# Performance work log

Hardware: AMD Instinct MI355X
Metric: run time of the kernel (lower is better)

Reference implementation:

```python
import jax, jax.numpy as jnp
import numpy as np

ENS, S_DIM, A_DIM, R_DIM, HID, LAYER_NUM = 7, 30, 8, 1, 200, 5
N_HID_LAYERS = LAYER_NUM - 2  # hidden->hidden Linear+Swish blocks


def swish(x):
    return x * jax.nn.sigmoid(x)


def setup_inputs() -> dict:
    key = jax.random.key(0)
    ks = jax.random.split(key, 14)
    N = 32768
    out_dim = S_DIM + R_DIM
    s = jax.random.normal(ks[0], (N, ENS, S_DIM), dtype=jnp.float32)
    a = jax.random.normal(ks[1], (N, ENS, A_DIM), dtype=jnp.float32)
    sc = 0.05
    W1 = jax.random.normal(ks[2], (ENS, S_DIM + A_DIM, HID), dtype=jnp.float32) * sc
    b1 = jax.random.normal(ks[3], (ENS, HID), dtype=jnp.float32) * sc
    Wh = jax.random.normal(ks[4], (N_HID_LAYERS, ENS, HID, HID), dtype=jnp.float32) * sc
    bh = jax.random.normal(ks[5], (N_HID_LAYERS, ENS, HID), dtype=jnp.float32) * sc
    Wmu = jax.random.normal(ks[6], (ENS, HID, out_dim), dtype=jnp.float32) * sc
    bmu = jax.random.normal(ks[7], (ENS, out_dim), dtype=jnp.float32) * sc
    Wsig = jax.random.normal(ks[8], (ENS, HID, out_dim), dtype=jnp.float32) * sc
    bsig = jax.random.normal(ks[9], (ENS, out_dim), dtype=jnp.float32) * sc
    max_lv_s = jnp.ones((1, S_DIM), dtype=jnp.float32) / 2.0
    min_lv_s = jnp.ones((1, S_DIM), dtype=jnp.float32) * -10.0
    max_lv_r = jnp.ones((1, R_DIM), dtype=jnp.float32) / 2.0
    min_lv_r = jnp.ones((1, R_DIM), dtype=jnp.float32) * -10.0
    return {"s": s, "a": a, "W1": W1, "b1": b1, "Wh": Wh, "bh": bh,
            "Wmu": Wmu, "bmu": bmu, "Wsig": Wsig, "bsig": bsig,
            "max_lv_s": max_lv_s, "min_lv_s": min_lv_s,
            "max_lv_r": max_lv_r, "min_lv_r": min_lv_r}


def reference(s, a, W1, b1, Wh, bh, Wmu, bmu, Wsig, bsig,
              max_lv_s, min_lv_s, max_lv_r, min_lv_r):
    # x: [N, E, s+a]; per-ensemble-member weights batched along E
    x = jnp.concatenate([s, a], axis=-1)
    h = swish(jnp.einsum('ned,edh->neh', x, W1) + b1)
    for i in range(Wh.shape[0]):
        h = swish(jnp.einsum('neh,ehk->nek', h, Wh[i]) + bh[i])
    mu = jnp.einsum('neh,eho->neo', h, Wmu) + bmu      # [N, E, s+r]
    sigma = jnp.einsum('neh,eho->neo', h, Wsig) + bsig  # raw logvar/2
    ds_mu, r_mu = mu[..., :S_DIM], mu[..., S_DIM:]
    ds_sg, r_sg = sigma[..., :S_DIM], sigma[..., S_DIM:]
    # soft clamping of log-variance, then exp
    ds_sg = (max_lv_s - jax.nn.softplus(max_lv_s - 2.0 * ds_sg)) / 2.0
    ds_sg = (min_lv_s + jax.nn.softplus(2.0 * ds_sg - min_lv_s)) / 2.0
    ds_sg = jnp.exp(ds_sg)
    r_sg = (max_lv_r - jax.nn.softplus(max_lv_r - 2.0 * r_sg)) / 2.0
    r_sg = (min_lv_r + jax.nn.softplus(2.0 * r_sg - min_lv_r)) / 2.0
    r_sg = jnp.exp(r_sg)
    return ((ds_mu, ds_sg), (r_mu, r_sg))
```

## Files before the change

### kernel.cpp

```cpp
#include <hip/hip_runtime.h>
#include <hip/hip_bf16.h>

#define ENS 7
#define SDIM 30
#define ADIM 8
#define DIN 38
#define HID 200
#define DOUT 31
#define NHL 3
#define HS 232
#define MT 64

typedef __bf16 bf16x8 __attribute__((ext_vector_type(8)));
typedef float f32x4 __attribute__((ext_vector_type(4)));

#define U_L1 13312
#define U_H 46592
#define OFF_HD2 (U_L1 + NHL * U_H)
#define PER_E (OFF_HD2 + 14336)
#define WS_TOTAL (ENS * PER_E)

__device__ __forceinline__ unsigned short f2bf(float f) {
    unsigned u = __float_as_uint(f);
    u += 0x7fffu + ((u >> 16) & 1u);
    return (unsigned short)(u >> 16);
}

__device__ __forceinline__ unsigned pk2(float a, float b) {
    __hip_bfloat162 h = __float22bfloat162_rn(make_float2(a, b));
    return *reinterpret_cast<unsigned*>(&h);
}

__device__ __forceinline__ float softplusf(float x) {
    return fmaxf(x, 0.f) + __logf(1.f + __expf(-fabsf(x)));
}

__global__ void prep_kernel(const float* __restrict__ W1, const float* __restrict__ Wh,
                            const float* __restrict__ Wmu, const float* __restrict__ Wsig,
                            unsigned short* __restrict__ ws) {
    int idx = blockIdx.x * 256 + threadIdx.x;
    if (idx >= WS_TOTAL) return;
    int e = idx / PER_E, r = idx % PER_E;
    int j = r & 7, lane = (r >> 3) & 63;
    int l16 = lane & 15, q = lane >> 4;
    float v = 0.f;
    if (r < U_L1) {
        int fi = r >> 9;
        int ct = fi >> 1, st = fi & 1;
        int k = st * 32 + q * 8 + j, n = ct * 16 + l16;
        if (k < DIN && n < HID) v = W1[(e * DIN + k) * HID + n];
    } else if (r < OFF_HD2) {
        int rh = r - U_L1;
        int l = rh / U_H, r2 = rh % U_H;
        int fi = r2 >> 9;
        int ct = fi / 7, st = fi % 7;
        int k = st * 32 + q * 8 + j, n = ct * 16 + l16;
        if (k < HID && n < HID) v = Wh[((l * ENS + e) * HID + (long)k) * HID + n];
    } else {
        int r2 = r - OFF_HD2;
        int fi = r2 >> 9;
        int ct = fi / 7, st = fi % 7;
        int k = st * 32 + q * 8 + j, n = ct * 16 + l16;
        if (k < HID) {
            if (n < DOUT) v = Wmu[(e * HID + k) * DOUT + n];
            else if (n >= 32 && n < 32 + DOUT) v = Wsig[(e * HID + k) * DOUT + (n - 32)];
        }
    }
    ws[idx] = f2bf(v);
}

template<int S, int NT>
__device__ __forceinline__ void runLayer(const unsigned short* __restrict__ gB,
                                         const unsigned short* hA,
                                         int wv, int lane, int l16, int quad,
                                         f32x4 acc[4][4]) {
#pragma unroll
    for (int r = 0; r < 4; r++)
#pragma unroll
        for (int j = 0; j < 4; j++) acc[r][j] = (f32x4){0.f, 0.f, 0.f, 0.f};

    const unsigned short* fp = gB + lane * 8;
    bf16x8 bcur[4], bnxt[4];
#pragma unroll
    for (int j = 0; j < 4; j++) {
        int ct = wv + 4 * j;
        if (ct < NT) bcur[j] = *((const bf16x8*)(fp + (ct * S) * 512));
    }
#pragma unroll
    for (int st = 0; st < S; ++st) {
        if (st + 1 < S) {
#pragma unroll
            for (int j = 0; j < 4; j++) {
                int ct = wv + 4 * j;
                if (ct < NT) bnxt[j] = *((const bf16x8*)(fp + (ct * S + st + 1) * 512));
            }
        }
        bf16x8 af[4];
#pragma unroll
        for (int r = 0; r < 4; r++)
            af[r] = *((const bf16x8*)(hA + (r * 16 + l16) * HS + st * 32 + quad * 8));
#pragma unroll
        for (int j = 0; j < 4; j++) {
            int ct = wv + 4 * j;
            if (ct < NT) {
#pragma unroll
                for (int r = 0; r < 4; r++)
                    acc[r][j] = __builtin_amdgcn_mfma_f32_16x16x32_bf16(bcur[j], af[r], acc[r][j], 0, 0, 0);
            }
        }
#pragma unroll
        for (int j = 0; j < 4; j++) bcur[j] = bnxt[j];
    }
}

__launch_bounds__(256, 3)
__global__ void ens_mlp_kernel(const float* __restrict__ s, const float* __restrict__ a,
                               const float* __restrict__ b1, const float* __restrict__ bh,
                               const float* __restrict__ bmu, const float* __restrict__ bsig,
                               const float* __restrict__ maxs, const float* __restrict__ mins,
                               const float* __restrict__ maxr, const float* __restrict__ minr,
                               const unsigned short* __restrict__ ws,
                               float* __restrict__ out, int N) {
    __shared__ unsigned short hA[MT * HS];

    const int tid = threadIdx.x;
    const int wv = tid >> 6, lane = tid & 63;
    const int quad = lane >> 4, l16 = lane & 15;
    const int bid = blockIdx.x;
    const int e = bid % ENS, n0 = (bid / ENS) * MT;

    for (int i = tid; i < MT * HS / 8; i += 256) ((uint4*)hA)[i] = make_uint4(0, 0, 0, 0);
    __syncthreads();

    {
        int m = tid & 63, cg = tid >> 6;
        long g = n0 + m;
        const float* srow = s + (g * ENS + e) * SDIM;
        const float* arow = a + (g * ENS + e) * ADIM;
#pragma unroll
        for (int k = 0; k < 10; k++) {
            int c = cg * 10 + k;
            if (c < DIN) {
                float v = (c < SDIM) ? srow[c] : arow[c - SDIM];
                hA[m * HS + c] = f2bf(v);
            }
        }
    }
    __syncthreads();

    f32x4 acc[4][4];

    auto epiH = [&](const float* bias) {
#pragma unroll
        for (int j = 0; j < 4; j++) {
            int ct = wv + 4 * j;
            if (ct < 13) {
                int col = ct * 16 + quad * 4;
                float4 bc4 = make_float4(0.f, 0.f, 0.f, 0.f);
                if (col < HID) bc4 = *((const float4*)(bias + col));
#pragma unroll
                for (int r = 0; r < 4; r++) {
                    int row = r * 16 + l16;
                    float v0 = acc[r][j][0] + bc4.x, v1 = acc[r][j][1] + bc4.y;
                    float v2 = acc[r][j][2] + bc4.z, v3 = acc[r][j][3] + bc4.w;
                    v0 *= __builtin_amdgcn_rcpf(1.f + __expf(-v0));
                    v1 *= __builtin_amdgcn_rcpf(1.f + __expf(-v1));
                    v2 *= __builtin_amdgcn_rcpf(1.f + __expf(-v2));
                    v3 *= __builtin_amdgcn_rcpf(1.f + __expf(-v3));
                    *((uint2*)(hA + row * HS + col)) = make_uint2(pk2(v0, v1), pk2(v2, v3));
                }
            }
        }
    };

    const unsigned short* we = ws + e * PER_E;

    runLayer<2, 13>(we, hA, wv, lane, l16, quad, acc);
    __syncthreads();
    epiH(b1 + e * HID);
    __syncthreads();
#pragma unroll
    for (int l = 0; l < NHL; l++) {
        runLayer<7, 13>(we + U_L1 + l * U_H, hA, wv, lane, l16, quad, acc);
        __syncthreads();
        epiH(bh + (l * ENS + e) * HID);
        __syncthreads();
    }
    runLayer<7, 4>(we + OFF_HD2, hA, wv, lane, l16, quad, acc);

    const long off1 = (long)N * ENS * SDIM;
    const long off2 = 2 * off1;
    const long off3 = off2 + (long)N * ENS;
    {
        const bool isSig = (wv >= 2);
        const int c0 = (wv & 1) * 16 + quad * 4;
        float bias_i[4], mx_i[4], mn_i[4];
#pragma unroll
        for (int i = 0; i < 4; i++) {
            int c = c0 + i;
            bias_i[i] = (c < DOUT) ? (isSig ? bsig : bmu)[e * DOUT + c] : 0.f;
            if (isSig) {
                mx_i[i] = (c < SDIM) ? maxs[c] : maxr[0];
                mn_i[i] = (c < SDIM) ? mins[c] : minr[0];
            }
        }
#pragma unroll
        for (int r = 0; r < 4; r++) {
            long g = n0 + r * 16 + l16;
            long rowbase = (g * ENS + e) * SDIM;
#pragma unroll
            for (int i = 0; i < 4; i++) {
                int c = c0 + i;
                if (c < DOUT) {
                    float v = acc[r][0][i] + bias_i[i];
                    if (!isSig) {
                        if (c < SDIM) out[rowbase + c] = v;
                        else out[off2 + g * ENS + e] = v;
                    } else {
                        v = 0.5f * (mx_i[i] - softplusf(mx_i[i] - 2.f * v));
                        v = 0.5f * (mn_i[i] + softplusf(2.f * v - mn_i[i]));
                        v = __expf(v);
                        if (c < SDIM) out[off1 + rowbase + c] = v;
                        else out[off3 + g * ENS + e] = v;
                    }
                }
            }
        }
    }
}

extern "C" void kernel_launch(void* const* d_in, const int* in_sizes, int n_in,
                              void* d_out, int out_size, void* d_ws, size_t ws_size,
                              hipStream_t stream) {
    const float* s    = (const float*)d_in[0];
    const float* a    = (const float*)d_in[1];
    const float* W1   = (const float*)d_in[2];
    const float* b1   = (const float*)d_in[3];
    const float* Wh   = (const float*)d_in[4];
    const float* bh   = (const float*)d_in[5];
    const float* Wmu  = (const float*)d_in[6];
    const float* bmu  = (const float*)d_in[7];
    const float* Wsig = (const float*)d_in[8];
    const float* bsig = (const float*)d_in[9];
    const float* maxs = (const float*)d_in[10];
    const float* mins = (const float*)d_in[11];
    const float* maxr = (const float*)d_in[12];
    const float* minr = (const float*)d_in[13];
    float* out = (float*)d_out;
    unsigned short* ws = (unsigned short*)d_ws;

    int N = in_sizes[0] / (ENS * SDIM);

    int prepBlocks = (WS_TOTAL + 255) / 256;
    prep_kernel<<<prepBlocks, 256, 0, stream>>>(W1, Wh, Wmu, Wsig, ws);

    int mainBlocks = (N / MT) * ENS;
    ens_mlp_kernel<<<mainBlocks, 256, 0, stream>>>(s, a, b1, bh, bmu, bsig,
                                                   maxs, mins, maxr, minr, ws, out, N);
}
```

Before: 264.3 us.

## Rebalance column tiles across waves and prefetch next layer weights across boundaries

```diff
diff --git a/kernel.cpp b/kernel.cpp
--- a/kernel.cpp
+++ b/kernel.cpp
@@ -69,51 +69,53 @@
     ws[idx] = f2bf(v);
 }
 
-template<int S, int NT>
-__device__ __forceinline__ void runLayer(const unsigned short* __restrict__ gB,
+template<int S, int OWN, bool SH, int NS, int NOWN, bool NSH>
+__device__ __forceinline__ void runLayer(const unsigned short* __restrict__ fo,
+                                         const unsigned short* __restrict__ fs,
+                                         const unsigned short* __restrict__ nfo,
+                                         const unsigned short* __restrict__ nfs,
                                          const unsigned short* hA,
-                                         int wv, int lane, int l16, int quad,
-                                         f32x4 acc[4][4]) {
+                                         int swv, int l16, int quad,
+                                         f32x4 (&accO)[4][3], f32x4& accS,
+                                         bf16x8 (&bq)[4]) {
 #pragma unroll
     for (int r = 0; r < 4; r++)
 #pragma unroll
-        for (int j = 0; j < 4; j++) acc[r][j] = (f32x4){0.f, 0.f, 0.f, 0.f};
-
-    const unsigned short* fp = gB + lane * 8;
-    bf16x8 bcur[4], bnxt[4];
-#pragma unroll
-    for (int j = 0; j < 4; j++) {
-        int ct = wv + 4 * j;
-        if (ct < NT) bcur[j] = *((const bf16x8*)(fp + (ct * S) * 512));
-    }
+        for (int c = 0; c < 3; c++) accO[r][c] = (f32x4){0.f, 0.f, 0.f, 0.f};
+    accS = (f32x4){0.f, 0.f, 0.f, 0.f};
+
 #pragma unroll
     for (int st = 0; st < S; ++st) {
+        bf16x8 bn[4];
         if (st + 1 < S) {
 #pragma unroll
-            for (int j = 0; j < 4; j++) {
-                int ct = wv + 4 * j;
-                if (ct < NT) bnxt[j] = *((const bf16x8*)(fp + (ct * S + st + 1) * 512));
-            }
+            for (int c = 0; c < OWN; c++) bn[c] = *((const bf16x8*)(fo + (c * S + st + 1) * 512));
+            if (SH) bn[3] = *((const bf16x8*)(fs + (st + 1) * 512));
+        } else if (NS > 0) {
+#pragma unroll
+            for (int c = 0; c < NOWN; c++) bn[c] = *((const bf16x8*)(nfo + (c * NS) * 512));
+            if (NSH) bn[3] = *((const bf16x8*)(nfs));
         }
         bf16x8 af[4];
 #pragma unroll
         for (int r = 0; r < 4; r++)
             af[r] = *((const bf16x8*)(hA + (r * 16 + l16) * HS + st * 32 + quad * 8));
-#pragma unroll
-        for (int j = 0; j < 4; j++) {
-            int ct = wv + 4 * j;
-            if (ct < NT) {
-#pragma unroll
-                for (int r = 0; r < 4; r++)
-                    acc[r][j] = __builtin_amdgcn_mfma_f32_16x16x32_bf16(bcur[j], af[r], acc[r][j], 0, 0, 0);
-            }
-        }
-#pragma unroll
-        for (int j = 0; j < 4; j++) bcur[j] = bnxt[j];
-    }
-}
-
-__launch_bounds__(256, 3)
+        bf16x8 afs;
+        if (SH) afs = *((const bf16x8*)(hA + (swv * 16 + l16) * HS + st * 32 + quad * 8));
+#pragma unroll
+        for (int c = 0; c < OWN; c++)
+#pragma unroll
+            for (int r = 0; r < 4; r++)
+                accO[r][c] = __builtin_amdgcn_mfma_f32_16x16x32_bf16(bq[c], af[r], accO[r][c], 0, 0, 0);
+        if (SH) accS = __builtin_amdgcn_mfma_f32_16x16x32_bf16(bq[3], afs, accS, 0, 0, 0);
+        if (st + 1 < S || NS > 0) {
+#pragma unroll
+            for (int c = 0; c < 4; c++) bq[c] = bn[c];
+        }
+    }
+}
+
+__launch_bounds__(256, 4)
 __global__ void ens_mlp_kernel(const float* __restrict__ s, const float* __restrict__ a,
                                const float* __restrict__ b1, const float* __restrict__ bh,
                                const float* __restrict__ bmu, const float* __restrict__ bsig,
@@ -126,6 +128,7 @@
     const int tid = threadIdx.x;
     const int wv = tid >> 6, lane = tid & 63;
     const int quad = lane >> 4, l16 = lane & 15;
+    const int swv = __builtin_amdgcn_readfirstlane(wv);
     const int bid = blockIdx.x;
     const int e = bid % ENS, n0 = (bid / ENS) * MT;
 
@@ -148,52 +151,82 @@
     }
     __syncthreads();
 
-    f32x4 acc[4][4];
+    const unsigned short* we = ws + e * PER_E;
+    const unsigned short* L1o = we + swv * 3 * 2 * 512 + lane * 8;
+    const unsigned short* L1s = we + 12 * 2 * 512 + lane * 8;
+    const unsigned short* H0o = we + U_L1 + swv * 3 * 7 * 512 + lane * 8;
+    const unsigned short* H0s = we + U_L1 + 12 * 7 * 512 + lane * 8;
+    const unsigned short* H1o = H0o + U_H;
+    const unsigned short* H1s = H0s + U_H;
+    const unsigned short* H2o = H1o + U_H;
+    const unsigned short* H2s = H1s + U_H;
+    const unsigned short* HDo = we + OFF_HD2 + swv * 7 * 512 + lane * 8;
+
+    f32x4 accO[4][3];
+    f32x4 accS;
+    bf16x8 bq[4];
 
     auto epiH = [&](const float* bias) {
 #pragma unroll
-        for (int j = 0; j < 4; j++) {
-            int ct = wv + 4 * j;
-            if (ct < 13) {
-                int col = ct * 16 + quad * 4;
-                float4 bc4 = make_float4(0.f, 0.f, 0.f, 0.f);
-                if (col < HID) bc4 = *((const float4*)(bias + col));
-#pragma unroll
-                for (int r = 0; r < 4; r++) {
-                    int row = r * 16 + l16;
-                    float v0 = acc[r][j][0] + bc4.x, v1 = acc[r][j][1] + bc4.y;
-                    float v2 = acc[r][j][2] + bc4.z, v3 = acc[r][j][3] + bc4.w;
-                    v0 *= __builtin_amdgcn_rcpf(1.f + __expf(-v0));
-                    v1 *= __builtin_amdgcn_rcpf(1.f + __expf(-v1));
-                    v2 *= __builtin_amdgcn_rcpf(1.f + __expf(-v2));
-                    v3 *= __builtin_amdgcn_rcpf(1.f + __expf(-v3));
-                    *((uint2*)(hA + row * HS + col)) = make_uint2(pk2(v0, v1), pk2(v2, v3));
-                }
-            }
+        for (int c = 0; c < 3; c++) {
+            int col = (3 * swv + c) * 16 + quad * 4;
+            float4 bc4 = *((const float4*)(bias + col));
+#pragma unroll
+            for (int r = 0; r < 4; r++) {
+                float v0 = accO[r][c][0] + bc4.x, v1 = accO[r][c][1] + bc4.y;
+                float v2 = accO[r][c][2] + bc4.z, v3 = accO[r][c][3] + bc4.w;
+                v0 *= __builtin_amdgcn_rcpf(1.f + __expf(-v0));
+                v1 *= __builtin_amdgcn_rcpf(1.f + __expf(-v1));
+                v2 *= __builtin_amdgcn_rcpf(1.f + __expf(-v2));
+                v3 *= __builtin_amdgcn_rcpf(1.f + __expf(-v3));
+                *((uint2*)(hA + (r * 16 + l16) * HS + col)) = make_uint2(pk2(v0, v1), pk2(v2, v3));
+            }
+        }
+        {
+            int col = 192 + quad * 4;
+            float4 bc4 = make_float4(0.f, 0.f, 0.f, 0.f);
+            if (col < HID) bc4 = *((const float4*)(bias + col));
+            float v0 = accS[0] + bc4.x, v1 = accS[1] + bc4.y;
+            float v2 = accS[2] + bc4.z, v3 = accS[3] + bc4.w;
+            v0 *= __builtin_amdgcn_rcpf(1.f + __expf(-v0));
+            v1 *= __builtin_amdgcn_rcpf(1.f + __expf(-v1));
+            v2 *= __builtin_amdgcn_rcpf(1.f + __expf(-v2));
+            v3 *= __builtin_amdgcn_rcpf(1.f + __expf(-v3));
+            *((uint2*)(hA + (swv * 16 + l16) * HS + col)) = make_uint2(pk2(v0, v1), pk2(v2, v3));
         }
     };
 
-    const unsigned short* we = ws + e * PER_E;
-
-    runLayer<2, 13>(we, hA, wv, lane, l16, quad, acc);
+#pragma unroll
+    for (int c = 0; c < 3; c++) bq[c] = *((const bf16x8*)(L1o + (c * 2) * 512));
+    bq[3] = *((const bf16x8*)(L1s));
+
+    runLayer<2, 3, true, 7, 3, true>(L1o, L1s, H0o, H0s, hA, swv, l16, quad, accO, accS, bq);
     __syncthreads();
     epiH(b1 + e * HID);
     __syncthreads();
-#pragma unroll
-    for (int l = 0; l < NHL; l++) {
-        runLayer<7, 13>(we + U_L1 + l * U_H, hA, wv, lane, l16, quad, acc);
-        __syncthreads();
-        epiH(bh + (l * ENS + e) * HID);
-        __syncthreads();
-    }
-    runLayer<7, 4>(we + OFF_HD2, hA, wv, lane, l16, quad, acc);
+    runLayer<7, 3, true, 7, 3, true>(H0o, H0s, H1o, H1s, hA, swv, l16, quad, accO, accS, bq);
+    __syncthreads();
+    epiH(bh + (0 * ENS + e) * HID);
+    __syncthreads();
+    runLayer<7, 3, true, 7, 3, true>(H1o, H1s, H2o, H2s, hA, swv, l16, quad, accO, accS, bq);
+    __syncthreads();
+    epiH(bh + (1 * ENS + e) * HID);
+    __syncthreads();
+    runLayer<7, 3, true, 7, 1, false>(H2o, H2s, HDo, (const unsigned short*)nullptr,
+                                      hA, swv, l16, quad, accO, accS, bq);
+    __syncthreads();
+    epiH(bh + (2 * ENS + e) * HID);
+    __syncthreads();
+    runLayer<7, 1, false, 0, 0, false>(HDo, (const unsigned short*)nullptr,
+                                       (const unsigned short*)nullptr, (const unsigned short*)nullptr,
+                                       hA, swv, l16, quad, accO, accS, bq);
 
     const long off1 = (long)N * ENS * SDIM;
     const long off2 = 2 * off1;
     const long off3 = off2 + (long)N * ENS;
     {
-        const bool isSig = (wv >= 2);
-        const int c0 = (wv & 1) * 16 + quad * 4;
+        const bool isSig = (swv >= 2);
+        const int c0 = (swv & 1) * 16 + quad * 4;
         float bias_i[4], mx_i[4], mn_i[4];
 #pragma unroll
         for (int i = 0; i < 4; i++) {
@@ -212,7 +245,7 @@
             for (int i = 0; i < 4; i++) {
                 int c = c0 + i;
                 if (c < DOUT) {
-                    float v = acc[r][0][i] + bias_i[i];
+                    float v = accO[r][0][i] + bias_i[i];
                     if (!isSig) {
                         if (c < SDIM) out[rowbase + c] = v;
                         else out[off2 + g * ENS + e] = v;
```

After: 264.7 us. No clear change (+0.1%).
